# Kernel optimization log

Measured on AMD Instinct MI355X. Metric: run time of the kernel, lower is better.

## Reference

```python
import jax, jax.numpy as jnp
import numpy as np

B, S, H, NH = 2, 2048, 1024, 16
D = H // NH
EPS = 1.1920929e-07  # torch fp32 finfo eps used by F.rms_norm default
ROPE_BASE = 10000.0


def setup_inputs() -> dict:
    key = jax.random.key(0)
    k0, k1, k2, k3 = jax.random.split(key, 4)
    return {
        "x": jax.random.normal(k0, (B, S, H), jnp.float32),
        "ve": jax.random.normal(k1, (B, S, H), jnp.float32),
        "W_qkv": jax.random.normal(k2, (3 * H, H), jnp.float32) * 0.02,
        "W_o": jax.random.normal(k3, (H, H), jnp.float32) * 0.02,
        "lambdas": jnp.array([0.5, 0.5], jnp.float32),
    }


def _rms_norm(x):
    # F.rms_norm without learnable weight, over last dim
    return x * jax.lax.rsqrt(jnp.mean(x * x, axis=-1, keepdims=True) + EPS)


def _rope(x):
    # x: [b, s, h, d]; rotate-half style RoPE matching the Rotary module
    d = x.shape[-1]
    inv_freq = (1.0 / ROPE_BASE) ** (jnp.arange(0, d, 2, dtype=jnp.float32) / d)
    t = jnp.arange(x.shape[1], dtype=jnp.float32)
    freqs = t[:, None] * inv_freq[None, :]          # [s, d/2]
    cos = jnp.cos(freqs)[None, :, None, :]
    sin = jnp.sin(freqs)[None, :, None, :]
    x1, x2 = jnp.split(x, 2, axis=-1)
    return jnp.concatenate([x1 * cos + x2 * sin, -x1 * sin + x2 * cos], axis=-1)


def reference(x, ve, W_qkv, W_o, lambdas):
    qkv = x @ W_qkv.T                                # [b, s, 3H]
    q, k, v = jnp.split(qkv, 3, axis=-1)
    rs = lambda a: a.reshape(B, S, NH, D)            # b s (h d) -> b s h d
    q, k, v = rs(q), rs(k), rs(v)
    q = _rope(_rms_norm(q))
    k = _rope(_rms_norm(k))
    v = lambdas[0] * v + lambdas[1] * rs(ve)         # value-lambda mix
    scale = 1.0 / jnp.sqrt(jnp.asarray(D, jnp.float32))  # flex_attention default
    scores = jnp.einsum('bqhd,bkhd->bhqk', q, k) * scale
    causal = jnp.tril(jnp.ones((S, S), bool))
    scores = jnp.where(causal[None, None], scores, jnp.asarray(-jnp.inf, scores.dtype))
    p = jax.nn.softmax(scores, axis=-1)
    a = jnp.einsum('bhqk,bkhd->bqhd', p, v).reshape(B, S, H)
    return a @ W_o.T
```

## Files before the change

kernel.cpp:

```cpp
#include <hip/hip_runtime.h>
#include <math.h>

typedef __bf16 bf16;
typedef __attribute__((ext_vector_type(8))) __bf16 bf16x8;
typedef __attribute__((ext_vector_type(4))) __bf16 bf16x4;
typedef __attribute__((ext_vector_type(4))) float f32x4;

#define B_  2
#define S_  2048
#define H_  1024
#define NH_ 16
#define D_  64

__device__ __forceinline__ f32x4 mfma16(bf16x8 a, bf16x8 b, f32x4 c) {
    return __builtin_amdgcn_mfma_f32_16x16x32_bf16(a, b, c, 0, 0, 0);
}

__device__ __forceinline__ void async16(void* lds, const void* g) {
    __builtin_amdgcn_global_load_lds(
        (const __attribute__((address_space(1))) unsigned int*)g,
        (__attribute__((address_space(3))) unsigned int*)lds, 16, 0, 0);
}

__global__ __launch_bounds__(256) void cvt_main(
    const float* __restrict__ x, const float* __restrict__ wqkv,
    bf16* __restrict__ xb, bf16* __restrict__ wqb, float2* __restrict__ tab)
{
    const int bid = blockIdx.x, tid = threadIdx.x;
    if (bid < 4096) {
        int i = bid * 256 + tid;
        f32x4 v = *(const f32x4*)(x + (size_t)i * 4);
        bf16x4 o; o[0]=(bf16)v[0]; o[1]=(bf16)v[1]; o[2]=(bf16)v[2]; o[3]=(bf16)v[3];
        *(bf16x4*)(xb + (size_t)i * 4) = o;
    } else if (bid < 7168) {
        int i = (bid - 4096) * 256 + tid;
        f32x4 v = *(const f32x4*)(wqkv + (size_t)i * 4);
        bf16x4 o; o[0]=(bf16)v[0]; o[1]=(bf16)v[1]; o[2]=(bf16)v[2]; o[3]=(bf16)v[3];
        *(bf16x4*)(wqb + (size_t)i * 4) = o;
    } else {
        int idx = (bid - 7168) * 256 + tid;
        int s = idx >> 5, i = idx & 31;
        float f = exp2f((float)i * (-13.287712379549449f / 32.0f));
        float sn, cs;
        sincosf((float)s * f, &sn, &cs);
        tab[idx] = make_float2(cs, sn);
    }
}

__global__ __launch_bounds__(256) void cvt_bf16(const float* __restrict__ src,
                                                bf16* __restrict__ dst, int n4) {
    int i = blockIdx.x * 256 + threadIdx.x;
    if (i >= n4) return;
    f32x4 v = *(const f32x4*)(src + (size_t)i * 4);
    bf16x4 o; o[0]=(bf16)v[0]; o[1]=(bf16)v[1]; o[2]=(bf16)v[2]; o[3]=(bf16)v[3];
    *(bf16x4*)(dst + (size_t)i * 4) = o;
}

template <int EPI>
__global__ __launch_bounds__(256) void gemm_bt(
    const bf16* __restrict__ A, const bf16* __restrict__ W,
    int M, int N, int K,
    float* __restrict__ outF,
    bf16* __restrict__ qb, bf16* __restrict__ kb, bf16* __restrict__ vtb,
    const float* __restrict__ ve, const float* __restrict__ lambdas,
    const float2* __restrict__ tab)
{
    __shared__ bf16 Al[128][32];
    __shared__ bf16 Bl[128][32];
    const int m0   = blockIdx.y * 128;
    const int n0   = blockIdx.x * 128;
    const int tid  = threadIdx.x;
    const int lane = tid & 63;
    const int w    = tid >> 6;
    const int quad = lane >> 4;
    const int l16  = lane & 15;
    const int wm   = (w >> 1) * 64;
    const int wn   = (w & 1) * 64;
    const int arow = lane >> 2;
    const int achk = (lane & 3) ^ ((lane >> 2) & 3);

    const f32x4 Z4 = {0.f, 0.f, 0.f, 0.f};
    f32x4 acc[4][4];
#pragma unroll
    for (int i = 0; i < 4; ++i)
#pragma unroll
        for (int j = 0; j < 4; ++j) acc[i][j] = Z4;

    for (int k0 = 0; k0 < K; k0 += 32) {
        const bf16* gB = W + (size_t)(n0 + w * 32 + arow) * K + k0 + achk * 8;
        async16(&Bl[w * 32][0], gB);
        async16(&Bl[w * 32 + 16][0], gB + (size_t)16 * K);
        const bf16* gA = A + (size_t)(m0 + w * 32 + arow) * K + k0 + achk * 8;
        async16(&Al[w * 32][0], gA);
        async16(&Al[w * 32 + 16][0], gA + (size_t)16 * K);
        __syncthreads();
        bf16x8 af[4], bfg[4];
#pragma unroll
        for (int i = 0; i < 4; ++i)
            af[i]  = *(const bf16x8*)&Al[wm + i * 16 + l16][(quad ^ (l16 & 3)) * 8];
#pragma unroll
        for (int j = 0; j < 4; ++j)
            bfg[j] = *(const bf16x8*)&Bl[wn + j * 16 + l16][(quad ^ (l16 & 3)) * 8];
#pragma unroll
        for (int i = 0; i < 4; ++i)
#pragma unroll
            for (int j = 0; j < 4; ++j)
                acc[i][j] = mfma16(af[i], bfg[j], acc[i][j]);
        __syncthreads();
    }

    if constexpr (EPI == 1) {
#pragma unroll
        for (int i = 0; i < 4; ++i)
#pragma unroll
            for (int j = 0; j < 4; ++j)
#pragma unroll
                for (int r = 0; r < 4; ++r) {
                    int m = m0 + wm + i * 16 + quad * 4 + r;
                    int n = n0 + wn + j * 16 + l16;
                    outF[(size_t)m * N + n] = acc[i][j][r];
                }
    } else {
        const int nbase = n0 + wn;
        const int which = nbase >> 10;
        const int h     = (nbase & (H_ - 1)) >> 6;
        if (which < 2) {
            bf16* dst = which ? kb : qb;
#pragma unroll
            for (int i = 0; i < 4; ++i) {
                float ss[4];
#pragma unroll
                for (int r = 0; r < 4; ++r)
                    ss[r] = acc[i][0][r] * acc[i][0][r] + acc[i][1][r] * acc[i][1][r]
                          + acc[i][2][r] * acc[i][2][r] + acc[i][3][r] * acc[i][3][r];
#pragma unroll
                for (int r = 0; r < 4; ++r) {
                    ss[r] += __shfl_xor(ss[r], 1);
                    ss[r] += __shfl_xor(ss[r], 2);
                    ss[r] += __shfl_xor(ss[r], 4);
                    ss[r] += __shfl_xor(ss[r], 8);
                }
#pragma unroll
                for (int r = 0; r < 4; ++r) {
                    int    m   = m0 + wm + i * 16 + quad * 4 + r;
                    int    bb  = m >> 11, s = m & (S_ - 1);
                    float  rms = rsqrtf(ss[r] * (1.0f / 64.0f) + 1.1920929e-07f);
                    float  x0 = acc[i][0][r] * rms, x1 = acc[i][1][r] * rms;
                    float  x2 = acc[i][2][r] * rms, x3 = acc[i][3][r] * rms;
                    float2 t0 = tab[(size_t)s * 32 + l16];
                    float2 t1 = tab[(size_t)s * 32 + 16 + l16];
                    bf16*  bp = dst + ((size_t)(bb * NH_ + h) * S_ + s) * D_;
                    bp[l16]      = (bf16)(x0 * t0.x + x2 * t0.y);
                    bp[16 + l16] = (bf16)(x1 * t1.x + x3 * t1.y);
                    bp[32 + l16] = (bf16)(x2 * t0.x - x0 * t0.y);
                    bp[48 + l16] = (bf16)(x3 * t1.x - x1 * t1.y);
                }
            }
        } else {
            const float l0 = lambdas[0], l1 = lambdas[1];
#pragma unroll
            for (int i = 0; i < 4; ++i) {
                const int m00 = m0 + wm + i * 16 + quad * 4;
                const int bb  = m00 >> 11, s = m00 & (S_ - 1);
#pragma unroll
                for (int j = 0; j < 4; ++j) {
                    const int d = j * 16 + l16;
                    bf16x4 pk;
#pragma unroll
                    for (int r = 0; r < 4; ++r) {
                        float vm = l0 * acc[i][j][r]
                                 + l1 * ve[(size_t)(m00 + r) * H_ + h * 64 + d];
                        pk[r] = (bf16)vm;
                    }
                    *(bf16x4*)&vtb[((size_t)(bb * NH_ + h) * D_ + d) * S_ + s] = pk;
                }
            }
        }
    }
}

__global__ __launch_bounds__(256) void attn(
    const bf16* __restrict__ Q, const bf16* __restrict__ Kg,
    const bf16* __restrict__ Vt, bf16* __restrict__ Og)
{
    __shared__ bf16 Kl[2][64][64];
    __shared__ bf16 Vl[2][64][64];
    __shared__ bf16 Pl[4][16][64];

    const int bh   = blockIdx.y;
    const int b    = bh >> 4;
    const int h    = bh & 15;
    const int qt   = gridDim.x - 1 - blockIdx.x;
    const int tid  = threadIdx.x;
    const int lane = tid & 63;
    const int w    = tid >> 6;
    const int quad = lane >> 4;
    const int l16  = lane & 15;
    const int l7   = l16 & 7;

    const bf16* Qp = Q  + (size_t)bh * S_ * D_;
    const bf16* Kp = Kg + (size_t)bh * S_ * D_;
    const bf16* Vp = Vt + (size_t)bh * D_ * S_;

    const int srow = lane >> 3;
    const int schk = (lane & 7) ^ (lane >> 3);
    const f32x4 Z4 = {0.f, 0.f, 0.f, 0.f};
    const float C1 = 0.18033688011112042f;
    const float C2 = -11.541560327111707f;

    const int qbase = qt * 64 + w * 16;
    const int qi    = qbase + l16;

    bf16x8 qf0 = *(const bf16x8*)(Qp + (size_t)(qbase + l16) * D_ + quad * 8);
    bf16x8 qf1 = *(const bf16x8*)(Qp + (size_t)(qbase + l16) * D_ + 32 + quad * 8);

    f32x4 of[4];
#pragma unroll
    for (int dt = 0; dt < 4; ++dt) of[dt] = Z4;
    float lsum = 0.f;

    auto stage = [&](int p, int kb0) {
        const bf16* gK = Kp + (size_t)(kb0 + w * 16 + srow) * D_ + schk * 8;
        async16(&Kl[p][w * 16][0], gK);
        async16(&Kl[p][w * 16 + 8][0], gK + (size_t)8 * D_);
        const bf16* gV = Vp + (size_t)(w * 16 + srow) * S_ + kb0 + schk * 8;
        async16(&Vl[p][w * 16][0], gV);
        async16(&Vl[p][w * 16 + 8][0], gV + (size_t)8 * S_);
    };

    stage(0, 0);
    const int nch = qt + 1;
    for (int c = 0; c < nch; ++c) {
        const int p   = c & 1;
        const int kb0 = c * 64;
        __syncthreads();
        if (c + 1 < nch) stage(p ^ 1, kb0 + 64);

        float ps = 0.f;
        if (c < qt) {
#pragma unroll
            for (int nt = 0; nt < 4; ++nt) {
                bf16x8 kf0 = *(const bf16x8*)&Kl[p][nt * 16 + l16][(quad ^ l7) * 8];
                bf16x8 kf1 = *(const bf16x8*)&Kl[p][nt * 16 + l16][((quad + 4) ^ l7) * 8];
                f32x4 sacc = Z4;
                sacc = mfma16(kf0, qf0, sacc);
                sacc = mfma16(kf1, qf1, sacc);
                bf16x4 pk;
#pragma unroll
                for (int r = 0; r < 4; ++r) {
                    float pv = exp2f(fmaf(sacc[r], C1, C2));
                    ps += pv;
                    pk[r] = (bf16)pv;
                }
                *(bf16x4*)&Pl[w][l16][((nt * 2 + (quad >> 1)) ^ l7) * 8 + (quad & 1) * 4] = pk;
            }
        } else {
#pragma unroll
            for (int nt = 0; nt < 4; ++nt) {
                bf16x8 kf0 = *(const bf16x8*)&Kl[p][nt * 16 + l16][(quad ^ l7) * 8];
                bf16x8 kf1 = *(const bf16x8*)&Kl[p][nt * 16 + l16][((quad + 4) ^ l7) * 8];
                f32x4 sacc = Z4;
                sacc = mfma16(kf0, qf0, sacc);
                sacc = mfma16(kf1, qf1, sacc);
                bf16x4 pk;
#pragma unroll
                for (int r = 0; r < 4; ++r) {
                    int   key = kb0 + nt * 16 + quad * 4 + r;
                    float pv  = (key <= qi) ? exp2f(fmaf(sacc[r], C1, C2)) : 0.f;
                    ps += pv;
                    pk[r] = (bf16)pv;
                }
                *(bf16x4*)&Pl[w][l16][((nt * 2 + (quad >> 1)) ^ l7) * 8 + (quad & 1) * 4] = pk;
            }
        }
        ps += __shfl_xor(ps, 16);
        ps += __shfl_xor(ps, 32);
        lsum += ps;

        bf16x8 pf0 = *(const bf16x8*)&Pl[w][l16][(quad ^ l7) * 8];
        bf16x8 pf1 = *(const bf16x8*)&Pl[w][l16][((quad + 4) ^ l7) * 8];
#pragma unroll
        for (int dt = 0; dt < 4; ++dt) {
            bf16x8 vf0 = *(const bf16x8*)&Vl[p][dt * 16 + l16][(quad ^ l7) * 8];
            bf16x8 vf1 = *(const bf16x8*)&Vl[p][dt * 16 + l16][((quad + 4) ^ l7) * 8];
            of[dt] = mfma16(pf0, vf0, of[dt]);
            of[dt] = mfma16(pf1, vf1, of[dt]);
        }
    }

#pragma unroll
    for (int r = 0; r < 4; ++r) {
        float ld = __shfl(lsum, quad * 4 + r);
        float rl = 1.0f / ld;
        int   qq = qbase + quad * 4 + r;
#pragma unroll
        for (int dt = 0; dt < 4; ++dt)
            Og[((size_t)(b * S_ + qq)) * H_ + h * D_ + dt * 16 + l16] =
                (bf16)(of[dt][r] * rl);
    }
}

extern "C" void kernel_launch(void* const* d_in, const int* in_sizes, int n_in,
                              void* d_out, int out_size, void* d_ws, size_t ws_size,
                              hipStream_t stream)
{
    const float* x       = (const float*)d_in[0];
    const float* ve      = (const float*)d_in[1];
    const float* Wqkv    = (const float*)d_in[2];
    const float* Wo      = (const float*)d_in[3];
    const float* lambdas = (const float*)d_in[4];
    float* out = (float*)d_out;

    char* od = (char*)d_out;
    char* ws = (char*)d_ws;
    const size_t MB = 1024 * 1024;
    bf16*   xb  = (bf16*)(od);
    bf16*   wqb = (bf16*)(od + 8 * MB);
    float2* tab = (float2*)(od + 14 * MB);
    bf16*   qb  = (bf16*)(ws);
    bf16*   kb  = (bf16*)(ws + 8 * MB);
    bf16*   vtb = (bf16*)(ws + 16 * MB);
    bf16*   ao  = (bf16*)(ws + 24 * MB);
    bf16*   wob = (bf16*)(ws);

    cvt_main<<<7424, 256, 0, stream>>>(x, Wqkv, xb, wqb, tab);
    gemm_bt<0><<<dim3(24, 32), 256, 0, stream>>>(
        xb, wqb, B_ * S_, 3 * H_, H_, nullptr, qb, kb, vtb, ve, lambdas, (const float2*)tab);
    attn<<<dim3(32, B_ * NH_), 256, 0, stream>>>(qb, kb, vtb, ao);
    cvt_bf16<<<1024, 256, 0, stream>>>(Wo, wob, (H_ * H_) / 4);
    gemm_bt<1><<<dim3(8, 32), 256, 0, stream>>>(
        ao, wob, B_ * S_, H_, H_, out, nullptr, nullptr, nullptr, nullptr, nullptr, nullptr);
}
```

Baseline: 245.0 us.

## Pair causal attention tiles per block, deepen GEMM K-step, narrow output GEMM tile

Each attention block now handles two query tiles, tile i and its mirror 31-i, so every block does the same total causal work, and the grid is halved to 16 blocks per head. The GEMM kernel loads 64-wide K slices per iteration, halving the number of barriers, and uses a wider XOR swizzle. The output projection uses 128x64 tiles, giving 512 blocks instead of 256 for better CU occupancy. The risks are fewer attention blocks (512 in total) and a larger shared-memory footprint per GEMM block.

```diff
diff --git a/kernel.cpp b/kernel.cpp
--- a/kernel.cpp
+++ b/kernel.cpp
@@ -56,7 +56,7 @@
     *(bf16x4*)(dst + (size_t)i * 4) = o;
 }
 
-template <int EPI>
+template <int EPI, int NT>
 __global__ __launch_bounds__(256) void gemm_bt(
     const bf16* __restrict__ A, const bf16* __restrict__ W,
     int M, int N, int K,
@@ -65,47 +65,65 @@
     const float* __restrict__ ve, const float* __restrict__ lambdas,
     const float2* __restrict__ tab)
 {
-    __shared__ bf16 Al[128][32];
-    __shared__ bf16 Bl[128][32];
+    constexpr int JN = NT / 32;
+    __shared__ bf16 Al[128][64];
+    __shared__ bf16 Bl[NT][64];
     const int m0   = blockIdx.y * 128;
-    const int n0   = blockIdx.x * 128;
+    const int n0   = blockIdx.x * NT;
     const int tid  = threadIdx.x;
     const int lane = tid & 63;
     const int w    = tid >> 6;
     const int quad = lane >> 4;
     const int l16  = lane & 15;
     const int wm   = (w >> 1) * 64;
-    const int wn   = (w & 1) * 64;
-    const int arow = lane >> 2;
-    const int achk = (lane & 3) ^ ((lane >> 2) & 3);
+    const int wn   = (w & 1) * (NT / 2);
+    const int r8   = lane >> 3;
+    const int cs   = ((lane & 7) ^ r8) * 8;
 
     const f32x4 Z4 = {0.f, 0.f, 0.f, 0.f};
-    f32x4 acc[4][4];
+    f32x4 acc[4][JN];
 #pragma unroll
     for (int i = 0; i < 4; ++i)
 #pragma unroll
-        for (int j = 0; j < 4; ++j) acc[i][j] = Z4;
-
-    for (int k0 = 0; k0 < K; k0 += 32) {
-        const bf16* gB = W + (size_t)(n0 + w * 32 + arow) * K + k0 + achk * 8;
-        async16(&Bl[w * 32][0], gB);
-        async16(&Bl[w * 32 + 16][0], gB + (size_t)16 * K);
-        const bf16* gA = A + (size_t)(m0 + w * 32 + arow) * K + k0 + achk * 8;
-        async16(&Al[w * 32][0], gA);
-        async16(&Al[w * 32 + 16][0], gA + (size_t)16 * K);
+        for (int j = 0; j < JN; ++j) acc[i][j] = Z4;
+
+    for (int k0 = 0; k0 < K; k0 += 64) {
+        {
+            const bf16* gA = A + (size_t)(m0 + w * 32 + r8) * K + k0 + cs;
+            async16(&Al[w * 32][0],      gA);
+            async16(&Al[w * 32 + 8][0],  gA + (size_t)8  * K);
+            async16(&Al[w * 32 + 16][0], gA + (size_t)16 * K);
+            async16(&Al[w * 32 + 24][0], gA + (size_t)24 * K);
+        }
+        if constexpr (NT == 128) {
+            const bf16* gB = W + (size_t)(n0 + w * 32 + r8) * K + k0 + cs;
+            async16(&Bl[w * 32][0],      gB);
+            async16(&Bl[w * 32 + 8][0],  gB + (size_t)8  * K);
+            async16(&Bl[w * 32 + 16][0], gB + (size_t)16 * K);
+            async16(&Bl[w * 32 + 24][0], gB + (size_t)24 * K);
+        } else {
+            const bf16* gB = W + (size_t)(n0 + w * 16 + r8) * K + k0 + cs;
+            async16(&Bl[w * 16][0],     gB);
+            async16(&Bl[w * 16 + 8][0], gB + (size_t)8 * K);
+        }
         __syncthreads();
-        bf16x8 af[4], bfg[4];
-#pragma unroll
-        for (int i = 0; i < 4; ++i)
-            af[i]  = *(const bf16x8*)&Al[wm + i * 16 + l16][(quad ^ (l16 & 3)) * 8];
-#pragma unroll
-        for (int j = 0; j < 4; ++j)
-            bfg[j] = *(const bf16x8*)&Bl[wn + j * 16 + l16][(quad ^ (l16 & 3)) * 8];
-#pragma unroll
-        for (int i = 0; i < 4; ++i)
-#pragma unroll
-            for (int j = 0; j < 4; ++j)
-                acc[i][j] = mfma16(af[i], bfg[j], acc[i][j]);
+#pragma unroll
+        for (int ks = 0; ks < 2; ++ks) {
+            bf16x8 af[4], bfg[JN];
+#pragma unroll
+            for (int i = 0; i < 4; ++i)
+                af[i] = *(const bf16x8*)
+                    &Al[wm + i * 16 + l16][(((ks << 2) + quad) ^ (l16 & 7)) * 8];
+#pragma unroll
+            for (int j = 0; j < JN; ++j)
+                bfg[j] = *(const bf16x8*)
+                    &Bl[wn + j * 16 + l16][(((ks << 2) + quad) ^ (l16 & 7)) * 8];
+#pragma unroll
+            for (int i = 0; i < 4; ++i)
+#pragma unroll
+                for (int j = 0; j < JN; ++j)
+                    acc[i][j] = mfma16(af[i], bfg[j], acc[i][j]);
+        }
         __syncthreads();
     }
 
@@ -113,7 +131,7 @@
 #pragma unroll
         for (int i = 0; i < 4; ++i)
 #pragma unroll
-            for (int j = 0; j < 4; ++j)
+            for (int j = 0; j < JN; ++j)
 #pragma unroll
                 for (int r = 0; r < 4; ++r) {
                     int m = m0 + wm + i * 16 + quad * 4 + r;
@@ -190,7 +208,6 @@
     const int bh   = blockIdx.y;
     const int b    = bh >> 4;
     const int h    = bh & 15;
-    const int qt   = gridDim.x - 1 - blockIdx.x;
     const int tid  = threadIdx.x;
     const int lane = tid & 63;
     const int w    = tid >> 6;
@@ -207,17 +224,6 @@
     const f32x4 Z4 = {0.f, 0.f, 0.f, 0.f};
     const float C1 = 0.18033688011112042f;
     const float C2 = -11.541560327111707f;
-
-    const int qbase = qt * 64 + w * 16;
-    const int qi    = qbase + l16;
-
-    bf16x8 qf0 = *(const bf16x8*)(Qp + (size_t)(qbase + l16) * D_ + quad * 8);
-    bf16x8 qf1 = *(const bf16x8*)(Qp + (size_t)(qbase + l16) * D_ + 32 + quad * 8);
-
-    f32x4 of[4];
-#pragma unroll
-    for (int dt = 0; dt < 4; ++dt) of[dt] = Z4;
-    float lsum = 0.f;
 
     auto stage = [&](int p, int kb0) {
         const bf16* gK = Kp + (size_t)(kb0 + w * 16 + srow) * D_ + schk * 8;
@@ -228,75 +234,90 @@
         async16(&Vl[p][w * 16 + 8][0], gV + (size_t)8 * S_);
     };
 
-    stage(0, 0);
-    const int nch = qt + 1;
-    for (int c = 0; c < nch; ++c) {
-        const int p   = c & 1;
-        const int kb0 = c * 64;
+    for (int half = 0; half < 2; ++half) {
+        const int qt    = half ? (31 - blockIdx.x) : blockIdx.x;
+        const int qbase = qt * 64 + w * 16;
+        const int qi    = qbase + l16;
+
+        bf16x8 qf0 = *(const bf16x8*)(Qp + (size_t)(qbase + l16) * D_ + quad * 8);
+        bf16x8 qf1 = *(const bf16x8*)(Qp + (size_t)(qbase + l16) * D_ + 32 + quad * 8);
+
+        f32x4 of[4];
+#pragma unroll
+        for (int dt = 0; dt < 4; ++dt) of[dt] = Z4;
+        float lsum = 0.f;
+
+        const int nch = qt + 1;
         __syncthreads();
-        if (c + 1 < nch) stage(p ^ 1, kb0 + 64);
-
-        float ps = 0.f;
-        if (c < qt) {
-#pragma unroll
-            for (int nt = 0; nt < 4; ++nt) {
-                bf16x8 kf0 = *(const bf16x8*)&Kl[p][nt * 16 + l16][(quad ^ l7) * 8];
-                bf16x8 kf1 = *(const bf16x8*)&Kl[p][nt * 16 + l16][((quad + 4) ^ l7) * 8];
-                f32x4 sacc = Z4;
-                sacc = mfma16(kf0, qf0, sacc);
-                sacc = mfma16(kf1, qf1, sacc);
-                bf16x4 pk;
-#pragma unroll
-                for (int r = 0; r < 4; ++r) {
-                    float pv = exp2f(fmaf(sacc[r], C1, C2));
-                    ps += pv;
-                    pk[r] = (bf16)pv;
-                }
-                *(bf16x4*)&Pl[w][l16][((nt * 2 + (quad >> 1)) ^ l7) * 8 + (quad & 1) * 4] = pk;
+        stage(0, 0);
+        for (int c = 0; c < nch; ++c) {
+            const int p   = c & 1;
+            const int kb0 = c * 64;
+            __syncthreads();
+            if (c + 1 < nch) stage(p ^ 1, kb0 + 64);
+
+            float ps = 0.f;
+            if (c < qt) {
+#pragma unroll
+                for (int nt = 0; nt < 4; ++nt) {
+                    bf16x8 kf0 = *(const bf16x8*)&Kl[p][nt * 16 + l16][(quad ^ l7) * 8];
+                    bf16x8 kf1 = *(const bf16x8*)&Kl[p][nt * 16 + l16][((quad + 4) ^ l7) * 8];
+                    f32x4 sacc = Z4;
+                    sacc = mfma16(kf0, qf0, sacc);
+                    sacc = mfma16(kf1, qf1, sacc);
+                    bf16x4 pk;
+#pragma unroll
+                    for (int r = 0; r < 4; ++r) {
+                        float pv = exp2f(fmaf(sacc[r], C1, C2));
+                        ps += pv;
+                        pk[r] = (bf16)pv;
+                    }
+                    *(bf16x4*)&Pl[w][l16][((nt * 2 + (quad >> 1)) ^ l7) * 8 + (quad & 1) * 4] = pk;
+                }
+            } else {
+#pragma unroll
+                for (int nt = 0; nt < 4; ++nt) {
+                    bf16x8 kf0 = *(const bf16x8*)&Kl[p][nt * 16 + l16][(quad ^ l7) * 8];
+                    bf16x8 kf1 = *(const bf16x8*)&Kl[p][nt * 16 + l16][((quad + 4) ^ l7) * 8];
+                    f32x4 sacc = Z4;
+                    sacc = mfma16(kf0, qf0, sacc);
+                    sacc = mfma16(kf1, qf1, sacc);
+                    bf16x4 pk;
+#pragma unroll
+                    for (int r = 0; r < 4; ++r) {
+                        int   key = kb0 + nt * 16 + quad * 4 + r;
+                        float pv  = (key <= qi) ? exp2f(fmaf(sacc[r], C1, C2)) : 0.f;
+                        ps += pv;
+                        pk[r] = (bf16)pv;
+                    }
+                    *(bf16x4*)&Pl[w][l16][((nt * 2 + (quad >> 1)) ^ l7) * 8 + (quad & 1) * 4] = pk;
+                }
             }
-        } else {
-#pragma unroll
-            for (int nt = 0; nt < 4; ++nt) {
-                bf16x8 kf0 = *(const bf16x8*)&Kl[p][nt * 16 + l16][(quad ^ l7) * 8];
-                bf16x8 kf1 = *(const bf16x8*)&Kl[p][nt * 16 + l16][((quad + 4) ^ l7) * 8];
-                f32x4 sacc = Z4;
-                sacc = mfma16(kf0, qf0, sacc);
-                sacc = mfma16(kf1, qf1, sacc);
-                bf16x4 pk;
-#pragma unroll
-                for (int r = 0; r < 4; ++r) {
-                    int   key = kb0 + nt * 16 + quad * 4 + r;
-                    float pv  = (key <= qi) ? exp2f(fmaf(sacc[r], C1, C2)) : 0.f;
-                    ps += pv;
-                    pk[r] = (bf16)pv;
-                }
-                *(bf16x4*)&Pl[w][l16][((nt * 2 + (quad >> 1)) ^ l7) * 8 + (quad & 1) * 4] = pk;
+            ps += __shfl_xor(ps, 16);
+            ps += __shfl_xor(ps, 32);
+            lsum += ps;
+
+            bf16x8 pf0 = *(const bf16x8*)&Pl[w][l16][(quad ^ l7) * 8];
+            bf16x8 pf1 = *(const bf16x8*)&Pl[w][l16][((quad + 4) ^ l7) * 8];
+#pragma unroll
+            for (int dt = 0; dt < 4; ++dt) {
+                bf16x8 vf0 = *(const bf16x8*)&Vl[p][dt * 16 + l16][(quad ^ l7) * 8];
+                bf16x8 vf1 = *(const bf16x8*)&Vl[p][dt * 16 + l16][((quad + 4) ^ l7) * 8];
+                of[dt] = mfma16(pf0, vf0, of[dt]);
+                of[dt] = mfma16(pf1, vf1, of[dt]);
             }
         }
-        ps += __shfl_xor(ps, 16);
-        ps += __shfl_xor(ps, 32);
-        lsum += ps;
-
-        bf16x8 pf0 = *(const bf16x8*)&Pl[w][l16][(quad ^ l7) * 8];
-        bf16x8 pf1 = *(const bf16x8*)&Pl[w][l16][((quad + 4) ^ l7) * 8];
-#pragma unroll
-        for (int dt = 0; dt < 4; ++dt) {
-            bf16x8 vf0 = *(const bf16x8*)&Vl[p][dt * 16 + l16][(quad ^ l7) * 8];
-            bf16x8 vf1 = *(const bf16x8*)&Vl[p][dt * 16 + l16][((quad + 4) ^ l7) * 8];
-            of[dt] = mfma16(pf0, vf0, of[dt]);
-            of[dt] = mfma16(pf1, vf1, of[dt]);
-        }
-    }
-
-#pragma unroll
-    for (int r = 0; r < 4; ++r) {
-        float ld = __shfl(lsum, quad * 4 + r);
-        float rl = 1.0f / ld;
-        int   qq = qbase + quad * 4 + r;
-#pragma unroll
-        for (int dt = 0; dt < 4; ++dt)
-            Og[((size_t)(b * S_ + qq)) * H_ + h * D_ + dt * 16 + l16] =
-                (bf16)(of[dt][r] * rl);
+
+#pragma unroll
+        for (int r = 0; r < 4; ++r) {
+            float ld = __shfl(lsum, quad * 4 + r);
+            float rl = 1.0f / ld;
+            int   qq = qbase + quad * 4 + r;
+#pragma unroll
+            for (int dt = 0; dt < 4; ++dt)
+                Og[((size_t)(b * S_ + qq)) * H_ + h * D_ + dt * 16 + l16] =
+                    (bf16)(of[dt][r] * rl);
+        }
     }
 }
 
@@ -324,10 +345,10 @@
     bf16*   wob = (bf16*)(ws);
 
     cvt_main<<<7424, 256, 0, stream>>>(x, Wqkv, xb, wqb, tab);
-    gemm_bt<0><<<dim3(24, 32), 256, 0, stream>>>(
+    gemm_bt<0, 128><<<dim3(24, 32), 256, 0, stream>>>(
         xb, wqb, B_ * S_, 3 * H_, H_, nullptr, qb, kb, vtb, ve, lambdas, (const float2*)tab);
-    attn<<<dim3(32, B_ * NH_), 256, 0, stream>>>(qb, kb, vtb, ao);
+    attn<<<dim3(16, B_ * NH_), 256, 0, stream>>>(qb, kb, vtb, ao);
     cvt_bf16<<<1024, 256, 0, stream>>>(Wo, wob, (H_ * H_) / 4);
-    gemm_bt<1><<<dim3(8, 32), 256, 0, stream>>>(
+    gemm_bt<1, 64><<<dim3(16, 32), 256, 0, stream>>>(
         ao, wob, B_ * S_, H_, H_, out, nullptr, nullptr, nullptr, nullptr, nullptr, nullptr);
 }
```

After: 208.1 us. -15.0%, faster.
